# Optimization experiments

Hardware: AMD Instinct MI355X
Metric: run time of the kernel (lower is better)

The kernel has to match this reference:

```python
import jax, jax.numpy as jnp
import numpy as np

HIDDEN = 512
NHEADS = 8
ALPHA = 0.1
NUM_HOP = 4
MASK_VAL = -16384.0
LN_EPS = 1e-5


def setup_inputs() -> dict:
    key = jax.random.key(0)
    ks = jax.random.split(key, 10)
    B, N, H = 8, 1024, HIDDEN
    s = 1.0 / np.sqrt(H)
    x = jax.random.normal(ks[0], (B, N, H), dtype=jnp.float32)
    adj = jax.random.randint(ks[1], (B, N, N), 0, 2, dtype=jnp.int32)
    Wq = jax.random.uniform(ks[2], (H, H), jnp.float32, -s, s)
    bq = jax.random.uniform(ks[3], (H,), jnp.float32, -s, s)
    Wk = jax.random.uniform(ks[4], (H, H), jnp.float32, -s, s)
    bk = jax.random.uniform(ks[5], (H,), jnp.float32, -s, s)
    Wv = jax.random.uniform(ks[6], (H, H), jnp.float32, -s, s)
    bv = jax.random.uniform(ks[7], (H,), jnp.float32, -s, s)
    gamma = jnp.ones((H,), jnp.float32)
    beta = jnp.zeros((H,), jnp.float32)
    return {"x": x, "adj": adj, "Wq": Wq, "bq": bq, "Wk": Wk, "bk": bk,
            "Wv": Wv, "bv": bv, "gamma": gamma, "beta": beta}


def reference(x, adj, Wq, bq, Wk, bk, Wv, bv, gamma, beta):
    B, N, H = x.shape
    u = H // NHEADS
    # torch Linear: y = x @ W^T + b
    q = x @ Wq.T + bq  # [B,N,H]
    k = x @ Wk.T + bk
    v = x @ Wv.T + bv
    # split hidden into contiguous head chunks (matches per-head slicing)
    qh = q.reshape(B, N, NHEADS, u).transpose(0, 2, 1, 3)  # [B,Hd,N,u]
    kh = k.reshape(B, N, NHEADS, u).transpose(0, 2, 1, 3)
    vh = v.reshape(B, N, NHEADS, u).transpose(0, 2, 1, 3)
    scores = jnp.einsum('bhnd,bhmd->bhnm', qh, kh)  # [B,Hd,N,N]
    mask = (adj == 0)[:, None, :, :]  # broadcast over heads
    scores = jnp.where(mask, MASK_VAL, scores)
    pros = jax.nn.softmax(scores, axis=-1)
    z_init = vh
    z = z_init
    for _ in range(NUM_HOP):
        z = (1.0 - ALPHA) * jnp.einsum('bhnm,bhmd->bhnd', pros, z) + ALPHA * z_init
    h_prime = z.transpose(0, 2, 1, 3).reshape(B, N, H)  # concat heads
    y = x + h_prime
    mu = jnp.mean(y, axis=-1, keepdims=True)
    var = jnp.mean((y - mu) ** 2, axis=-1, keepdims=True)
    return (y - mu) / jnp.sqrt(var + LN_EPS) * gamma + beta
```

## Files before the change

kernel.cpp:

```cpp
#include <hip/hip_runtime.h>
#include <hip/hip_bf16.h>

#define BB 8
#define NN 1024
#define HH 512
#define NHEADS 8
#define UU 64

typedef __attribute__((ext_vector_type(8))) short short8;
typedef __attribute__((ext_vector_type(4))) float f32x4;
typedef __attribute__((ext_vector_type(16))) float f32x16;
typedef unsigned short u16;
typedef unsigned char u8;

__device__ inline float b2f(unsigned short u) {
    union { float f; unsigned int i; } c; c.i = ((unsigned int)u) << 16; return c.f;
}
__device__ inline unsigned short f2b(float f) {
    __hip_bfloat16 h = __float2bfloat16(f);
    return *reinterpret_cast<unsigned short*>(&h);
}
__device__ inline unsigned int pkbf(float a, float b) {
    unsigned int r;
    asm("v_cvt_pk_bf16_f32 %0, %1, %2" : "=v"(r) : "v"(a), "v"(b));
    return r;
}
__device__ inline float upk_lo(unsigned int u) {
    union { float f; unsigned int i; } c; c.i = u << 16; return c.f;
}
__device__ inline float upk_hi(unsigned int u) {
    union { float f; unsigned int i; } c; c.i = u & 0xffff0000u; return c.f;
}
__device__ inline void gl_lds16(const void* g, void* l) {
    __builtin_amdgcn_global_load_lds(
        (const __attribute__((address_space(1))) unsigned int*)g,
        (__attribute__((address_space(3))) unsigned int*)l, 16, 0, 0);
}

__global__ __launch_bounds__(256) void cvt_w(
    const float* __restrict__ Wq, const float* __restrict__ Wk,
    const float* __restrict__ Wv, u16* __restrict__ Wb)
{
    const int which = blockIdx.y;
    const float* src = which == 0 ? Wq : (which == 1 ? Wk : Wv);
    u16* dst = Wb + (size_t)which * HH * HH;
    const int base = (blockIdx.x * 256 + threadIdx.x) * 8;
    const float4* sp = (const float4*)&src[base];
    float4 a = sp[0], b = sp[1];
    short8 o;
    o[0] = (short)f2b(a.x); o[1] = (short)f2b(a.y);
    o[2] = (short)f2b(a.z); o[3] = (short)f2b(a.w);
    o[4] = (short)f2b(b.x); o[5] = (short)f2b(b.y);
    o[6] = (short)f2b(b.z); o[7] = (short)f2b(b.w);
    *(short8*)&dst[base] = o;
}

__global__ __launch_bounds__(256) void cvt_x(
    const float* __restrict__ x, u16* __restrict__ xb)
{
    const int base = (blockIdx.x * 256 + threadIdx.x) * 8;
    const float4* sp = (const float4*)&x[base];
    float4 a = sp[0], b = sp[1];
    short8 o;
    o[0] = (short)f2b(a.x); o[1] = (short)f2b(a.y);
    o[2] = (short)f2b(a.z); o[3] = (short)f2b(a.w);
    o[4] = (short)f2b(b.x); o[5] = (short)f2b(b.y);
    o[6] = (short)f2b(b.z); o[7] = (short)f2b(b.w);
    *(short8*)&xb[base] = o;
}

__global__ __launch_bounds__(256) void adj_pack(
    const int* __restrict__ adj, unsigned int* __restrict__ adjpT)
{
    const int wave = threadIdx.x >> 6, lane = threadIdx.x & 63;
    const int row = blockIdx.x * 4 + wave;
    const int b = row >> 10, r = row & 1023;
    const int* ar = adj + (size_t)row * NN;
    unsigned int* ob = adjpT + (((size_t)b) << 15) + r;
    #pragma unroll
    for (int it = 0; it < 16; ++it) {
        int a = ar[it * 64 + lane];
        unsigned long long m = __ballot(a != 0);
        if (lane == 0) {
            ob[(size_t)(2 * it)     << 10] = (unsigned int)m;
            ob[(size_t)(2 * it + 1) << 10] = (unsigned int)(m >> 32);
        }
    }
}

__global__ __launch_bounds__(256, 4) void qkv_gemm(
    const u16* __restrict__ xb, const u16* __restrict__ Wb,
    const float* __restrict__ bq, const float* __restrict__ bk,
    const float* __restrict__ bv,
    u16* __restrict__ q, u16* __restrict__ k, u16* __restrict__ v)
{
    const int which = blockIdx.z;
    const u16* W      = Wb + (size_t)which * HH * HH;
    const float* bias = which == 0 ? bq : (which == 1 ? bk : bv);
    u16* out          = which == 0 ? q  : (which == 1 ? k  : v);

    const int tid = threadIdx.x;
    const int wave = tid >> 6, lane = tid & 63;
    const int ln = lane & 15, quad = lane >> 4;
    const int wr = (wave >> 1) * 64, wc = (wave & 1) * 64;
    const int rowbase = blockIdx.x * 128, colbase = blockIdx.y * 128;

    __shared__ __align__(16) char smem[128 * 136 * 2];
    u16* As = (u16*)smem;
    u16* Bs = (u16*)(smem + 128 * 32 * 2);
    u16* Cs = (u16*)smem;

    f32x4 acc[4][4];
    #pragma unroll
    for (int ri = 0; ri < 4; ++ri)
        #pragma unroll
        for (int ci = 0; ci < 4; ++ci) acc[ri][ci] = (f32x4){0.f, 0.f, 0.f, 0.f};

    const int lr = lane >> 2;
    const int sg = lane & 3;

    for (int kk = 0; kk < HH; kk += 32) {
        __syncthreads();
        #pragma unroll
        for (int i = 0; i < 2; ++i) {
            int r = wave * 32 + i * 16 + lr;
            gl_lds16(&xb[(size_t)(rowbase + r) * HH + kk + sg * 8],
                     (char*)As + (wave * 32 + i * 16) * 64);
            gl_lds16(&W[(size_t)(colbase + r) * HH + kk + sg * 8],
                     (char*)Bs + (wave * 32 + i * 16) * 64);
        }
        __syncthreads();

        short8 bfr[4];
        #pragma unroll
        for (int ci = 0; ci < 4; ++ci)
            bfr[ci] = *(const short8*)&Bs[(wc + ci * 16 + ln) * 32 + quad * 8];
        #pragma unroll
        for (int ri = 0; ri < 4; ++ri) {
            short8 af = *(const short8*)&As[(wr + ri * 16 + ln) * 32 + quad * 8];
            #pragma unroll
            for (int ci = 0; ci < 4; ++ci)
                acc[ri][ci] = __builtin_amdgcn_mfma_f32_16x16x32_bf16(af, bfr[ci], acc[ri][ci], 0, 0, 0);
        }
    }

    __syncthreads();
    #pragma unroll
    for (int ci = 0; ci < 4; ++ci) {
        int col = wc + ci * 16 + ln;
        float bb = bias[colbase + col];
        #pragma unroll
        for (int ri = 0; ri < 4; ++ri) {
            #pragma unroll
            for (int r = 0; r < 4; ++r) {
                int row = wr + ri * 16 + quad * 4 + r;
                Cs[row * 136 + col] = f2b(acc[ri][ci][r] + bb);
            }
        }
    }
    __syncthreads();
    {
        int row = tid >> 1, half = tid & 1;
        int gcol0 = colbase + half * 64;
        int hh = gcol0 >> 6;
        int grow = rowbase + row;
        int bidx = grow >> 10, n = grow & 1023;
        u16* op = &out[(((size_t)(bidx * NHEADS + hh)) * NN + n) * UU];
        const u16* cp = &Cs[row * 136 + half * 64];
        #pragma unroll
        for (int j = 0; j < 8; ++j)
            *(short8*)(op + j * 8) = *(const short8*)(cp + j * 8);
    }
}

__global__ __launch_bounds__(256) void vt8(
    const u16* __restrict__ v, u8* __restrict__ v8t)
{
    const int bh = blockIdx.x >> 2, part = blockIdx.x & 3;
    const int t = threadIdx.x;
    const size_t hd = (size_t)bh << 16;
    __shared__ u16 tile[64][72];

    for (int chunk = part * 4; chunk < part * 4 + 4; ++chunk) {
        const int n0 = chunk * 64;
        const int r = t >> 2, cs = t & 3;
        const u16* vp = &v[((size_t)bh * NN + n0 + r) * UU + cs * 16];
        short8 a = *(const short8*)vp;
        short8 b8 = *(const short8*)(vp + 8);
        #pragma unroll
        for (int j = 0; j < 8; ++j) {
            tile[r][cs * 16 + j] = (u16)a[j];
            tile[r][cs * 16 + 8 + j] = (u16)b8[j];
        }
        __syncthreads();
        const int c = t & 63, qt = t >> 6;
        unsigned int w[4];
        #pragma unroll
        for (int g = 0; g < 4; ++g) {
            float f0 = b2f(tile[qt * 16 + g * 4 + 0][c]);
            float f1 = b2f(tile[qt * 16 + g * 4 + 1][c]);
            float f2 = b2f(tile[qt * 16 + g * 4 + 2][c]);
            float f3 = b2f(tile[qt * 16 + g * 4 + 3][c]);
            int lo = __builtin_amdgcn_cvt_pk_fp8_f32(f0, f1, 0, false);
            w[g] = (unsigned int)__builtin_amdgcn_cvt_pk_fp8_f32(f2, f3, lo, true);
        }
        uint4 o; o.x = w[0]; o.y = w[1]; o.z = w[2]; o.w = w[3];
        *(uint4*)&v8t[hd + (size_t)c * 1024 + n0 + qt * 16] = o;
        __syncthreads();
    }
}

__device__ inline f32x16 score_tile(const u16* kp, const short8* qf)
{
    short8 kf[4];
    #pragma unroll
    for (int f = 0; f < 4; ++f) kf[f] = *(const short8*)(kp + f * 16);
    f32x16 acc;
    #pragma unroll
    for (int j = 0; j < 16; ++j) acc[j] = 0.f;
    #pragma unroll
    for (int f = 0; f < 4; ++f)
        acc = __builtin_amdgcn_mfma_f32_32x32x16_bf16(kf[f], qf[f], acc, 0, 0, 0);
    return acc;
}

__global__ __launch_bounds__(512, 4) void scores_softmax(
    const u16* __restrict__ q, const u16* __restrict__ kmat,
    const unsigned int* __restrict__ adjpT, u8* __restrict__ P8)
{
    const int gid = blockIdx.x;
    const int j = gid >> 3;
    const int h = gid & 7;
    const int b = j >> 5;
    const int bx = j & 31;
    const int bh = b * NHEADS + h;

    const int tid = threadIdx.x;
    const int kq = tid >> 6, lane = tid & 63;
    const int l31 = lane & 31, hi = lane >> 5;
    const int n = bx * 32 + l31;
    const int kt0 = kq * 4;

    __shared__ float rs[8][32];

    short8 qf[4];
    const u16* qp = &q[((size_t)bh * NN + n) * UU + hi * 8];
    #pragma unroll
    for (int f = 0; f < 4; ++f) qf[f] = *(const short8*)(qp + f * 16);

    const u16* kbase = kmat + (size_t)bh * NN * UU + (size_t)(kt0 * 32 + l31) * UU + hi * 8;
    const unsigned int* mbase = adjpT + (((size_t)b) << 15) + n;

    unsigned int mv[4];
    #pragma unroll
    for (int i = 0; i < 4; ++i)
        mv[i] = mbase[(size_t)(kt0 + i) << 10] >> (4 * hi);

    const float L2E = 1.442695041f;
    const float C0 = -46.16624f;
    const float CM = -100000.0f;

    unsigned int eb[4][4][2];
    float rs0 = 0.f, rs1 = 0.f, rs2 = 0.f, rs3 = 0.f;
    #pragma unroll
    for (int i = 0; i < 4; ++i) {
        f32x16 acc = score_tile(kbase + (size_t)i * (32 * UU), qf);
        const unsigned int m2 = mv[i];
        #pragma unroll
        for (int g = 0; g < 4; ++g) {
            float e[4];
            #pragma unroll
            for (int r = 0; r < 4; ++r) {
                const int koff = r + 8 * g;
                float addv = ((m2 >> koff) & 1u) ? C0 : CM;
                e[r] = __builtin_amdgcn_exp2f(fmaf(L2E, acc[g * 4 + r], addv));
            }
            if (g == 0) rs0 += (e[0] + e[1]) + (e[2] + e[3]);
            else if (g == 1) rs1 += (e[0] + e[1]) + (e[2] + e[3]);
            else if (g == 2) rs2 += (e[0] + e[1]) + (e[2] + e[3]);
            else rs3 += (e[0] + e[1]) + (e[2] + e[3]);
            eb[i][g][0] = pkbf(e[0], e[1]);
            eb[i][g][1] = pkbf(e[2], e[3]);
        }
    }
    float rsum = (rs0 + rs1) + (rs2 + rs3);
    rsum += __shfl_xor(rsum, 32);
    if (lane < 32) rs[kq][lane] = rsum;
    __syncthreads();
    const float total = ((rs[0][l31] + rs[1][l31]) + (rs[2][l31] + rs[3][l31]))
                      + ((rs[4][l31] + rs[5][l31]) + (rs[6][l31] + rs[7][l31]));
    const float scl = 16.0f / total;

    u8* pb = P8 + (((size_t)bh) << 20) + (size_t)(n >> 4) * 16384
           + (n & 15) * 32 + hi * 16;
    #pragma unroll
    for (int i = 0; i < 4; ++i) {
        unsigned int dw[4];
        #pragma unroll
        for (int g = 0; g < 4; ++g) {
            float e0 = upk_lo(eb[i][g][0]) * scl;
            float e1 = upk_hi(eb[i][g][0]) * scl;
            float e2 = upk_lo(eb[i][g][1]) * scl;
            float e3 = upk_hi(eb[i][g][1]) * scl;
            int lo = __builtin_amdgcn_cvt_pk_fp8_f32(e0, e1, 0, false);
            dw[g] = (unsigned int)__builtin_amdgcn_cvt_pk_fp8_f32(e2, e3, lo, true);
        }
        unsigned int sendA = hi ? dw[0] : dw[2];
        unsigned int sendB = hi ? dw[1] : dw[3];
        unsigned int recvA = (unsigned int)__shfl_xor((int)sendA, 32);
        unsigned int recvB = (unsigned int)__shfl_xor((int)sendB, 32);
        uint4 o;
        o.x = hi ? recvA : dw[0];
        o.y = hi ? dw[2] : recvA;
        o.z = hi ? recvB : dw[1];
        o.w = hi ? dw[3] : recvB;
        *(uint4*)(pb + (size_t)(kt0 + i) * 512) = o;
    }
}

__global__ __launch_bounds__(512) void hop(
    const u8* __restrict__ P8, const u8* __restrict__ z8in,
    const u16* __restrict__ v, u8* __restrict__ z8out,
    u16* __restrict__ zbf_out, int last)
{
    const int b = blockIdx.z, h = blockIdx.y, rt = blockIdx.x;
    const int bh = b * NHEADS + h;
    const int tid = threadIdx.x;
    const int wave = tid >> 6, lane = tid & 63;
    const int ln = lane & 15, quad = lane >> 4;
    const int wrow = rt * 128 + wave * 16;

    __shared__ __align__(16) u8 zt[64 * 1040];

    const u8* zg = z8in + ((size_t)bh << 16);
    #pragma unroll
    for (int i = 0; i < 8; ++i) {
        int c = wave * 8 + i;
        gl_lds16(zg + (size_t)c * 1024 + lane * 16, (char*)zt + c * 1040);
    }

    const u8* pt = P8 + ((size_t)bh << 20) + (size_t)(rt * 8 + wave) * 16384
                 + ln * 32 + quad * 8;
    long pa[4];
    #pragma unroll
    for (int i = 0; i < 4; ++i) pa[i] = *(const long*)(pt + i * 512);

    __syncthreads();

    f32x4 acc[4];
    #pragma unroll
    for (int ci = 0; ci < 4; ++ci) acc[ci] = (f32x4){0.f, 0.f, 0.f, 0.f};

    #pragma unroll
    for (int kc = 0; kc < 32; ++kc) {
        long a = pa[kc & 3];
        if (kc + 4 < 32) pa[kc & 3] = *(const long*)(pt + (kc + 4) * 512);
        int kk = kc * 32;
        #pragma unroll
        for (int ci = 0; ci < 4; ++ci) {
            long bz = *(const long*)&zt[(ci * 16 + ln) * 1040 + kk + quad * 8];
            acc[ci] = __builtin_amdgcn_mfma_f32_16x16x32_fp8_fp8(a, bz, acc[ci], 0, 0, 0);
        }
    }

    if (last) {
        #pragma unroll
        for (int ci = 0; ci < 4; ++ci) {
            int col = ci * 16 + ln;
            #pragma unroll
            for (int r = 0; r < 4; ++r) {
                int row = wrow + quad * 4 + r;
                float vv = b2f(v[((size_t)bh * NN + row) * UU + col]);
                zbf_out[((size_t)(b * NN + row)) * HH + h * UU + col]
                    = f2b(0.05625f * acc[ci][r] + 0.1f * vv);
            }
        }
    } else {
        u8* zo = z8out + ((size_t)bh << 16);
        #pragma unroll
        for (int ci = 0; ci < 4; ++ci) {
            int col = ci * 16 + ln;
            float zv[4];
            #pragma unroll
            for (int r = 0; r < 4; ++r) {
                int row = wrow + quad * 4 + r;
                float vv = b2f(v[((size_t)bh * NN + row) * UU + col]);
                zv[r] = 0.05625f * acc[ci][r] + 0.1f * vv;
            }
            int lo = __builtin_amdgcn_cvt_pk_fp8_f32(zv[0], zv[1], 0, false);
            unsigned int dw = (unsigned int)__builtin_amdgcn_cvt_pk_fp8_f32(zv[2], zv[3], lo, true);
            *(unsigned int*)&zo[(size_t)col * 1024 + wrow + quad * 4] = dw;
        }
    }
}

__global__ __launch_bounds__(256) void resid_ln(
    const float* __restrict__ x, const u16* __restrict__ z,
    const float* __restrict__ gamma, const float* __restrict__ beta,
    float* __restrict__ out)
{
    const int r = blockIdx.x * 4 + (threadIdx.x >> 6);
    const int lane = threadIdx.x & 63;
    const size_t base = (size_t)r * HH + lane * 8;

    const float4* xp = (const float4*)&x[base];
    float4 x0 = xp[0], x1 = xp[1];
    short8 zv = *(const short8*)&z[base];
    float y[8];
    y[0] = x0.x + b2f((u16)zv[0]); y[1] = x0.y + b2f((u16)zv[1]);
    y[2] = x0.z + b2f((u16)zv[2]); y[3] = x0.w + b2f((u16)zv[3]);
    y[4] = x1.x + b2f((u16)zv[4]); y[5] = x1.y + b2f((u16)zv[5]);
    y[6] = x1.z + b2f((u16)zv[6]); y[7] = x1.w + b2f((u16)zv[7]);

    float s = 0.f, sq = 0.f;
    #pragma unroll
    for (int j = 0; j < 8; ++j) { s += y[j]; sq += y[j] * y[j]; }
    #pragma unroll
    for (int off = 32; off >= 1; off >>= 1) {
        s  += __shfl_xor(s, off);
        sq += __shfl_xor(sq, off);
    }
    const float mu = s * (1.0f / HH);
    const float var = sq * (1.0f / HH) - mu * mu;
    const float rstd = rsqrtf(var + 1e-5f);

    const float4* gp = (const float4*)&gamma[lane * 8];
    const float4* bp = (const float4*)&beta[lane * 8];
    float4 g0 = gp[0], g1 = gp[1], b0 = bp[0], b1 = bp[1];

    float4 o0, o1;
    o0.x = (y[0] - mu) * rstd * g0.x + b0.x;
    o0.y = (y[1] - mu) * rstd * g0.y + b0.y;
    o0.z = (y[2] - mu) * rstd * g0.z + b0.z;
    o0.w = (y[3] - mu) * rstd * g0.w + b0.w;
    o1.x = (y[4] - mu) * rstd * g1.x + b1.x;
    o1.y = (y[5] - mu) * rstd * g1.y + b1.y;
    o1.z = (y[6] - mu) * rstd * g1.z + b1.z;
    o1.w = (y[7] - mu) * rstd * g1.w + b1.w;
    float4* op = (float4*)&out[base];
    op[0] = o0; op[1] = o1;
}

extern "C" void kernel_launch(void* const* d_in, const int* in_sizes, int n_in,
                              void* d_out, int out_size, void* d_ws, size_t ws_size,
                              hipStream_t stream)
{
    const float* x   = (const float*)d_in[0];
    const int* adj   = (const int*)d_in[1];
    const float* Wq  = (const float*)d_in[2];
    const float* bq  = (const float*)d_in[3];
    const float* Wk  = (const float*)d_in[4];
    const float* bk  = (const float*)d_in[5];
    const float* Wv  = (const float*)d_in[6];
    const float* bv  = (const float*)d_in[7];
    const float* gamma = (const float*)d_in[8];
    const float* beta  = (const float*)d_in[9];
    float* out = (float*)d_out;

    const size_t E = (size_t)BB * NN * HH;
    u16* ws16 = (u16*)d_ws;
    u16* xb = ws16;
    u16* q  = ws16 + E;
    u16* k  = ws16 + 2 * E;
    u16* v  = ws16 + 3 * E;
    u16* za = ws16 + 4 * E;
    u16* Wb = ws16 + 5 * E;
    u8* base8 = (u8*)(ws16 + 5 * E + 786432);
    u8* P8  = base8;
    u8* z8a = base8 + ((size_t)64 << 20);
    u8* z8b = z8a + ((size_t)4 << 20);
    u8* v8t = z8b + ((size_t)4 << 20);
    unsigned int* adjpT = (unsigned int*)(v8t + ((size_t)4 << 20));

    cvt_x<<<dim3(2048), 256, 0, stream>>>(x, xb);
    cvt_w<<<dim3(128, 3), 256, 0, stream>>>(Wq, Wk, Wv, Wb);
    adj_pack<<<dim3(2048), 256, 0, stream>>>(adj, adjpT);
    qkv_gemm<<<dim3(64, 4, 3), 256, 0, stream>>>(xb, Wb, bq, bk, bv, q, k, v);
    vt8<<<dim3(256), 256, 0, stream>>>(v, v8t);
    scores_softmax<<<dim3(2048), 512, 0, stream>>>(q, k, adjpT, P8);
    hop<<<dim3(8, NHEADS, BB), 512, 0, stream>>>(P8, v8t, v, z8a, za, 0);
    hop<<<dim3(8, NHEADS, BB), 512, 0, stream>>>(P8, z8a, v, z8b, za, 0);
    hop<<<dim3(8, NHEADS, BB), 512, 0, stream>>>(P8, z8b, v, z8a, za, 0);
    hop<<<dim3(8, NHEADS, BB), 512, 0, stream>>>(P8, z8a, v, z8b, za, 1);
    resid_ln<<<dim3(2048), 256, 0, stream>>>(x, za, gamma, beta, out);
}
```

Measured before the change: 268.6 us.

## Merge conversion kernels, double-buffer QKV GEMM loads, widen vt8 grid

Three unrelated tweaks. The x and weight bf16 conversion kernels become one launch, which saves a launch gap. The QKV GEMM K-loop now double-buffers its LDS tiles, so the next slice's global-to-LDS load is issued while the current slice runs MFMA. The vt8 transpose launches one block per 64-row chunk instead of looping over four chunks, which gives it more parallelism. The double-buffered GEMM uses 32KB of its roughly 34KB LDS buffer and keeps a single barrier per iteration, which could race with the asynchronous LDS loads.

```diff
diff --git a/kernel.cpp b/kernel.cpp
--- a/kernel.cpp
+++ b/kernel.cpp
@@ -37,14 +37,26 @@
         (__attribute__((address_space(3))) unsigned int*)l, 16, 0, 0);
 }
 
-__global__ __launch_bounds__(256) void cvt_w(
-    const float* __restrict__ Wq, const float* __restrict__ Wk,
-    const float* __restrict__ Wv, u16* __restrict__ Wb)
-{
-    const int which = blockIdx.y;
-    const float* src = which == 0 ? Wq : (which == 1 ? Wk : Wv);
-    u16* dst = Wb + (size_t)which * HH * HH;
-    const int base = (blockIdx.x * 256 + threadIdx.x) * 8;
+__global__ __launch_bounds__(256) void cvt_all(
+    const float* __restrict__ x, const float* __restrict__ Wq,
+    const float* __restrict__ Wk, const float* __restrict__ Wv,
+    u16* __restrict__ xb, u16* __restrict__ Wb)
+{
+    const int gid = blockIdx.x;
+    const float* src;
+    u16* dst;
+    int base;
+    if (gid < 2048) {
+        src = x; dst = xb;
+        base = (gid * 256 + threadIdx.x) * 8;
+    } else {
+        const int g = gid - 2048;
+        const int which = g >> 7;
+        const int slice = g & 127;
+        src = which == 0 ? Wq : (which == 1 ? Wk : Wv);
+        dst = Wb + (size_t)which * HH * HH;
+        base = (slice * 256 + threadIdx.x) * 8;
+    }
     const float4* sp = (const float4*)&src[base];
     float4 a = sp[0], b = sp[1];
     short8 o;
@@ -55,20 +67,6 @@
     *(short8*)&dst[base] = o;
 }
 
-__global__ __launch_bounds__(256) void cvt_x(
-    const float* __restrict__ x, u16* __restrict__ xb)
-{
-    const int base = (blockIdx.x * 256 + threadIdx.x) * 8;
-    const float4* sp = (const float4*)&x[base];
-    float4 a = sp[0], b = sp[1];
-    short8 o;
-    o[0] = (short)f2b(a.x); o[1] = (short)f2b(a.y);
-    o[2] = (short)f2b(a.z); o[3] = (short)f2b(a.w);
-    o[4] = (short)f2b(b.x); o[5] = (short)f2b(b.y);
-    o[6] = (short)f2b(b.z); o[7] = (short)f2b(b.w);
-    *(short8*)&xb[base] = o;
-}
-
 __global__ __launch_bounds__(256) void adj_pack(
     const int* __restrict__ adj, unsigned int* __restrict__ adjpT)
 {
@@ -106,8 +104,6 @@
     const int rowbase = blockIdx.x * 128, colbase = blockIdx.y * 128;
 
     __shared__ __align__(16) char smem[128 * 136 * 2];
-    u16* As = (u16*)smem;
-    u16* Bs = (u16*)(smem + 128 * 32 * 2);
     u16* Cs = (u16*)smem;
 
     f32x4 acc[4][4];
@@ -119,17 +115,25 @@
     const int lr = lane >> 2;
     const int sg = lane & 3;
 
-    for (int kk = 0; kk < HH; kk += 32) {
-        __syncthreads();
+    auto STAGE = [&](int buf, int kk) {
+        char* Ab = smem + buf * 16384;
+        char* Bb = smem + 8192 + buf * 16384;
         #pragma unroll
         for (int i = 0; i < 2; ++i) {
             int r = wave * 32 + i * 16 + lr;
             gl_lds16(&xb[(size_t)(rowbase + r) * HH + kk + sg * 8],
-                     (char*)As + (wave * 32 + i * 16) * 64);
+                     Ab + (wave * 32 + i * 16) * 64);
             gl_lds16(&W[(size_t)(colbase + r) * HH + kk + sg * 8],
-                     (char*)Bs + (wave * 32 + i * 16) * 64);
-        }
+                     Bb + (wave * 32 + i * 16) * 64);
+        }
+    };
+
+    STAGE(0, 0);
+    for (int s = 0; s < 16; ++s) {
         __syncthreads();
+        if (s < 15) STAGE((s + 1) & 1, (s + 1) * 32);
+        const u16* As = (const u16*)(smem + (s & 1) * 16384);
+        const u16* Bs = (const u16*)(smem + 8192 + (s & 1) * 16384);
 
         short8 bfr[4];
         #pragma unroll
@@ -176,38 +180,35 @@
 __global__ __launch_bounds__(256) void vt8(
     const u16* __restrict__ v, u8* __restrict__ v8t)
 {
-    const int bh = blockIdx.x >> 2, part = blockIdx.x & 3;
+    const int bh = blockIdx.x >> 4, chunk = blockIdx.x & 15;
     const int t = threadIdx.x;
     const size_t hd = (size_t)bh << 16;
     __shared__ u16 tile[64][72];
 
-    for (int chunk = part * 4; chunk < part * 4 + 4; ++chunk) {
-        const int n0 = chunk * 64;
-        const int r = t >> 2, cs = t & 3;
-        const u16* vp = &v[((size_t)bh * NN + n0 + r) * UU + cs * 16];
-        short8 a = *(const short8*)vp;
-        short8 b8 = *(const short8*)(vp + 8);
-        #pragma unroll
-        for (int j = 0; j < 8; ++j) {
-            tile[r][cs * 16 + j] = (u16)a[j];
-            tile[r][cs * 16 + 8 + j] = (u16)b8[j];
-        }
-        __syncthreads();
-        const int c = t & 63, qt = t >> 6;
-        unsigned int w[4];
-        #pragma unroll
-        for (int g = 0; g < 4; ++g) {
-            float f0 = b2f(tile[qt * 16 + g * 4 + 0][c]);
-            float f1 = b2f(tile[qt * 16 + g * 4 + 1][c]);
-            float f2 = b2f(tile[qt * 16 + g * 4 + 2][c]);
-            float f3 = b2f(tile[qt * 16 + g * 4 + 3][c]);
-            int lo = __builtin_amdgcn_cvt_pk_fp8_f32(f0, f1, 0, false);
-            w[g] = (unsigned int)__builtin_amdgcn_cvt_pk_fp8_f32(f2, f3, lo, true);
-        }
-        uint4 o; o.x = w[0]; o.y = w[1]; o.z = w[2]; o.w = w[3];
-        *(uint4*)&v8t[hd + (size_t)c * 1024 + n0 + qt * 16] = o;
-        __syncthreads();
-    }
+    const int n0 = chunk * 64;
+    const int r = t >> 2, cs = t & 3;
+    const u16* vp = &v[((size_t)bh * NN + n0 + r) * UU + cs * 16];
+    short8 a = *(const short8*)vp;
+    short8 b8 = *(const short8*)(vp + 8);
+    #pragma unroll
+    for (int j = 0; j < 8; ++j) {
+        tile[r][cs * 16 + j] = (u16)a[j];
+        tile[r][cs * 16 + 8 + j] = (u16)b8[j];
+    }
+    __syncthreads();
+    const int c = t & 63, qt = t >> 6;
+    unsigned int w[4];
+    #pragma unroll
+    for (int g = 0; g < 4; ++g) {
+        float f0 = b2f(tile[qt * 16 + g * 4 + 0][c]);
+        float f1 = b2f(tile[qt * 16 + g * 4 + 1][c]);
+        float f2 = b2f(tile[qt * 16 + g * 4 + 2][c]);
+        float f3 = b2f(tile[qt * 16 + g * 4 + 3][c]);
+        int lo = __builtin_amdgcn_cvt_pk_fp8_f32(f0, f1, 0, false);
+        w[g] = (unsigned int)__builtin_amdgcn_cvt_pk_fp8_f32(f2, f3, lo, true);
+    }
+    uint4 o; o.x = w[0]; o.y = w[1]; o.z = w[2]; o.w = w[3];
+    *(uint4*)&v8t[hd + (size_t)c * 1024 + n0 + qt * 16] = o;
 }
 
 __device__ inline f32x16 score_tile(const u16* kp, const short8* qf)
@@ -472,11 +473,10 @@
     u8* v8t = z8b + ((size_t)4 << 20);
     unsigned int* adjpT = (unsigned int*)(v8t + ((size_t)4 << 20));
 
-    cvt_x<<<dim3(2048), 256, 0, stream>>>(x, xb);
-    cvt_w<<<dim3(128, 3), 256, 0, stream>>>(Wq, Wk, Wv, Wb);
+    cvt_all<<<dim3(2432), 256, 0, stream>>>(x, Wq, Wk, Wv, xb, Wb);
     adj_pack<<<dim3(2048), 256, 0, stream>>>(adj, adjpT);
     qkv_gemm<<<dim3(64, 4, 3), 256, 0, stream>>>(xb, Wb, bq, bk, bv, q, k, v);
-    vt8<<<dim3(256), 256, 0, stream>>>(v, v8t);
+    vt8<<<dim3(1024), 256, 0, stream>>>(v, v8t);
     scores_softmax<<<dim3(2048), 512, 0, stream>>>(q, k, adjpT, P8);
     hop<<<dim3(8, NHEADS, BB), 512, 0, stream>>>(P8, v8t, v, z8a, za, 0);
     hop<<<dim3(8, NHEADS, BB), 512, 0, stream>>>(P8, z8a, v, z8b, za, 0);
```

Measured after the change: 265.0 us. Within noise of the previous version (-1.3%).
